# Kernel optimization log

Hardware: AMD Instinct MI355X
Metric: run time of the kernel (lower is better)

## Reference

```python
import jax, jax.numpy as jnp
import numpy as np

B, H, N, D = 4, 16, 4096, 64
M = 266  # nb_features = int(D * ln(D))
KERNEL_EPS = 1e-4


def _gaussian_orthogonal_random_matrix(nb_rows, nb_cols, rng):
    # Faithful to gaussian_orthogonal_random_matrix with scaling=0.
    blocks = []
    for _ in range(nb_rows // nb_cols):
        q, _ = np.linalg.qr(rng.standard_normal((nb_cols, nb_cols)))
        blocks.append(q.T)
    rem = nb_rows - (nb_rows // nb_cols) * nb_cols
    if rem > 0:
        q, _ = np.linalg.qr(rng.standard_normal((nb_cols, nb_cols)))
        blocks.append(q.T[:rem])
    final = np.concatenate(blocks, axis=0)
    mult = np.linalg.norm(rng.standard_normal((nb_rows, nb_cols)), axis=1)
    return (mult[:, None] * final).astype(np.float32)


def setup_inputs() -> dict:
    key = jax.random.key(0)
    kq, kk, kv = jax.random.split(key, 3)
    q = jax.random.normal(kq, (B, H, N, D), dtype=jnp.float32)
    k = jax.random.normal(kk, (B, H, N, D), dtype=jnp.float32)
    v = jax.random.normal(kv, (B, H, N, D), dtype=jnp.float32)
    proj = jnp.asarray(_gaussian_orthogonal_random_matrix(M, D, np.random.default_rng(0)))
    return {"q": q, "k": k, "v": v, "projection_matrix": proj}


def _softmax_kernel(x, proj, is_query):
    d = x.shape[-1]
    data_normalizer = d ** (-0.25)
    ratio = proj.shape[0] ** (-0.5)
    # [b,h,n,m]
    data_dash = jnp.einsum("bhnd,md->bhnm", data_normalizer * x, proj)
    diag = jnp.sum(x * x, axis=-1, keepdims=True) * 0.5 * (data_normalizer ** 2)
    if is_query:
        mx = jax.lax.stop_gradient(jnp.max(data_dash, axis=-1, keepdims=True))
    else:
        mx = jax.lax.stop_gradient(jnp.max(data_dash, axis=(-1, -2), keepdims=True))
    return ratio * (jnp.exp(data_dash - diag - mx) + KERNEL_EPS)


def _linear_attention(q, k, v):
    k_cumsum = jnp.sum(k, axis=-2)                       # [b,h,m]
    D_ = jnp.einsum("bhnm,bhm->bhn", q, k_cumsum)
    D_inv = 1.0 / jnp.where(D_ == 0, 1e-5, D_)
    context = jnp.einsum("bhnm,bhne->bhme", k, v)        # [b,h,m,e]
    return jnp.einsum("bhme,bhnm,bhn->bhne", context, q, D_inv)


def reference(q, k, v, projection_matrix):
    qp = _softmax_kernel(q, projection_matrix, is_query=True)
    kp = _softmax_kernel(k, projection_matrix, is_query=False)
    return _linear_attention(qp, kp, v)
```

## Files before the change

kernel.cpp:

```cpp
#include <hip/hip_runtime.h>
#include <math.h>


#define BH 64
#define NTOK 4096
#define DIM 64
#define MF 266
#define MPAD 272
#define NCH 4
#define CHROWS 1024
#define SUBS 16
#define RATIO 0.06131393394849658f
#define DNORM 0.35355339059327373f
#define DIAGC 0.0625f
#define L2E   1.4426950408889634f
#define KEPS 1e-4f

#define PSTR 72
#define QSTR 296

typedef _Float16 half8 __attribute__((ext_vector_type(8)));
typedef _Float16 half4 __attribute__((ext_vector_type(4)));
typedef __fp16 fp16x2 __attribute__((ext_vector_type(2)));
typedef float floatx4 __attribute__((ext_vector_type(4)));
typedef short short8 __attribute__((ext_vector_type(8)));
typedef short short4s __attribute__((ext_vector_type(4)));

__device__ __forceinline__ short f2h_bits(float f) {
    union { _Float16 h; short s; } u; u.h = (_Float16)f; return u.s;
}
__device__ __forceinline__ float h2f(short s) {
    union { short s; _Float16 h; } u; u.s = s; return (float)u.h;
}
__device__ __forceinline__ unsigned cvt_pk_bf16(float lo, float hi) {
    unsigned r;
    asm("v_cvt_pk_bf16_f32 %0, %1, %2" : "=v"(r) : "v"(lo), "v"(hi));
    return r;
}
__device__ __forceinline__ float fexp2(float x) {
    float r;
    asm("v_exp_f32 %0, %1" : "=v"(r) : "v"(x));
    return r;
}
__device__ __forceinline__ unsigned encf(float f) {
    unsigned u = __float_as_uint(f);
    return (u & 0x80000000u) ? ~u : (u | 0x80000000u);
}
__device__ __forceinline__ float decf(unsigned u) {
    u = (u & 0x80000000u) ? (u & 0x7FFFFFFFu) : ~u;
    return __uint_as_float(u);
}

__global__ __launch_bounds__(512, 4)
void k_pass(const float* __restrict__ kin, const float* __restrict__ vin,
            const float* __restrict__ proj, float* __restrict__ A0p,
            float* __restrict__ S0p, unsigned int* __restrict__ gmax)
{
    __shared__ __align__(16) short kL[2][64 * PSTR];
    __shared__ __align__(16) short vT[2][64 * PSTR];
    __shared__ float diagL[2][64];
    __shared__ __align__(16) short epS[16][16 * PSTR];

    const int tid = threadIdx.x;
    const int l = tid & 63, w = tid >> 6;
    const int c = tid & 15, g = (tid >> 4) & 3;
    const int h    = blockIdx.x >> 8;
    const int rest = blockIdx.x & 255;
    const int bh   = rest >> 2;
    const int ch   = rest & 3;
    const int nT = (h == 1 && w == 0) ? 2 : 1;
    const int t0 = (h == 0) ? w : (8 + w);

    const float PSC = DNORM * L2E;
    half8 pj0[2], pj1[2];
    #pragma unroll
    for (int it = 0; it < 2; ++it) {
        half8 z;
        #pragma unroll
        for (int j = 0; j < 8; ++j) z[j] = (_Float16)0.f;
        pj0[it] = z; pj1[it] = z;
        const int t = it ? 16 : t0;
        const int f = 16 * t + c;
        if (it < nT && f < MF) {
            const float* ps = proj + (size_t)f * 64 + 8 * g;
            float4 x0 = *(const float4*)ps;
            float4 x1 = *(const float4*)(ps + 4);
            float4 x2 = *(const float4*)(ps + 32);
            float4 x3 = *(const float4*)(ps + 36);
            half8 b0, b1;
            b0[0]=(_Float16)(PSC*x0.x); b0[1]=(_Float16)(PSC*x0.y);
            b0[2]=(_Float16)(PSC*x0.z); b0[3]=(_Float16)(PSC*x0.w);
            b0[4]=(_Float16)(PSC*x1.x); b0[5]=(_Float16)(PSC*x1.y);
            b0[6]=(_Float16)(PSC*x1.z); b0[7]=(_Float16)(PSC*x1.w);
            b1[0]=(_Float16)(PSC*x2.x); b1[1]=(_Float16)(PSC*x2.y);
            b1[2]=(_Float16)(PSC*x2.z); b1[3]=(_Float16)(PSC*x2.w);
            b1[4]=(_Float16)(PSC*x3.x); b1[5]=(_Float16)(PSC*x3.y);
            b1[6]=(_Float16)(PSC*x3.z); b1[7]=(_Float16)(PSC*x3.w);
            pj0[it] = b0; pj1[it] = b1;
        }
    }

    const float* kb = kin + ((size_t)bh * NTOK + (size_t)ch * CHROWS) * DIM;
    const float* vb = vin + ((size_t)bh * NTOK + (size_t)ch * CHROWS) * DIM;

    const int srow = 8 * w + (l >> 3);
    const int sd0  = (l & 7) * 8;
    const int vrow = l;
    const int ve0  = 8 * w;

    floatx4 acc[2][4];
    #pragma unroll
    for (int it = 0; it < 2; ++it)
        #pragma unroll
        for (int et = 0; et < 4; ++et) {
            acc[it][et][0]=0.f; acc[it][et][1]=0.f; acc[it][et][2]=0.f; acc[it][et][3]=0.f;
        }
    float s0acc[2] = {0.f, 0.f};
    float dmax = -3.0e38f;

    float4 ka0, ka1, va0, va1;

    auto issue_loads = [&](int s) {
        const float* ks = kb + (size_t)(64 * s + srow) * DIM + sd0;
        ka0 = *(const float4*)ks;
        ka1 = *(const float4*)(ks + 4);
        const float* vs = vb + (size_t)(64 * s + vrow) * DIM + ve0;
        va0 = *(const float4*)vs;
        va1 = *(const float4*)(vs + 4);
    };

    auto stage_write = [&](int buf) {
        union { fp16x2 h2[4]; short8 s8; } uk;
        uk.h2[0] = __builtin_amdgcn_cvt_pkrtz(ka0.x, ka0.y);
        uk.h2[1] = __builtin_amdgcn_cvt_pkrtz(ka0.z, ka0.w);
        uk.h2[2] = __builtin_amdgcn_cvt_pkrtz(ka1.x, ka1.y);
        uk.h2[3] = __builtin_amdgcn_cvt_pkrtz(ka1.z, ka1.w);
        *(short8*)&kL[buf][srow * PSTR + sd0] = uk.s8;
        float ds2 = ka0.x*ka0.x + ka0.y*ka0.y + ka0.z*ka0.z + ka0.w*ka0.w
                  + ka1.x*ka1.x + ka1.y*ka1.y + ka1.z*ka1.z + ka1.w*ka1.w;
        ds2 += __shfl_xor(ds2, 1);
        ds2 += __shfl_xor(ds2, 2);
        ds2 += __shfl_xor(ds2, 4);
        if ((l & 7) == 0) diagL[buf][srow] = ds2 * (DIAGC * L2E);
        unsigned pv0 = cvt_pk_bf16(va0.x, va0.y);
        unsigned pv1 = cvt_pk_bf16(va0.z, va0.w);
        unsigned pv2 = cvt_pk_bf16(va1.x, va1.y);
        unsigned pv3 = cvt_pk_bf16(va1.z, va1.w);
        vT[buf][(ve0 + 0) * PSTR + vrow] = (short)(pv0 & 0xFFFF);
        vT[buf][(ve0 + 1) * PSTR + vrow] = (short)(pv0 >> 16);
        vT[buf][(ve0 + 2) * PSTR + vrow] = (short)(pv1 & 0xFFFF);
        vT[buf][(ve0 + 3) * PSTR + vrow] = (short)(pv1 >> 16);
        vT[buf][(ve0 + 4) * PSTR + vrow] = (short)(pv2 & 0xFFFF);
        vT[buf][(ve0 + 5) * PSTR + vrow] = (short)(pv2 >> 16);
        vT[buf][(ve0 + 6) * PSTR + vrow] = (short)(pv3 & 0xFFFF);
        vT[buf][(ve0 + 7) * PSTR + vrow] = (short)(pv3 >> 16);
    };

    issue_loads(0);
    stage_write(0);
    __syncthreads();

    for (int s = 0; s < SUBS; ++s) {
        const int cur = s & 1;
        const bool more = (s + 1 < SUBS);
        if (more) issue_loads(s + 1);

        #pragma unroll
        for (int nt = 0; nt < 4; ++nt) {
            const half8 a0 = *(const half8*)&kL[cur][(16 * nt + c) * PSTR + 8 * g];
            const half8 a1 = *(const half8*)&kL[cur][(16 * nt + c) * PSTR + 8 * g + 32];
            const float4 dg4 = *(const float4*)&diagL[cur][16 * nt + 4 * g];
            const float dgr[4] = {dg4.x, dg4.y, dg4.z, dg4.w};
            #pragma unroll
            for (int it = 0; it < 2; ++it) {
                if (it < nT) {
                    floatx4 d = {0.f, 0.f, 0.f, 0.f};
                    d = __builtin_amdgcn_mfma_f32_16x16x32_f16(a0, pj0[it], d, 0, 0, 0);
                    d = __builtin_amdgcn_mfma_f32_16x16x32_f16(a1, pj1[it], d, 0, 0, 0);
                    const bool t16 = (it == 1);
                    float ev[4];
                    #pragma unroll
                    for (int r = 0; r < 4; ++r) {
                        const float ddv = d[r];
                        if (!t16 || c < 10) dmax = fmaxf(dmax, ddv);
                        float e = fexp2(ddv - dgr[r]);
                        if (t16 && c == 15) e = 1.0f;
                        s0acc[it] += e;
                        ev[r] = e;
                    }
                    uint2 pk;
                    pk.x = cvt_pk_bf16(ev[0], ev[1]);
                    pk.y = cvt_pk_bf16(ev[2], ev[3]);
                    *(uint2*)&epS[2 * w + it][c * PSTR + 16 * nt + 4 * g] = pk;
                }
            }
        }

        #pragma unroll
        for (int ntp = 0; ntp < 2; ++ntp) {
            const short8 bq0 = *(const short8*)&epS[2 * w][c * PSTR + 32 * ntp + 8 * g];
            short8 bq1;
            if (nT == 2) bq1 = *(const short8*)&epS[2 * w + 1][c * PSTR + 32 * ntp + 8 * g];
            #pragma unroll
            for (int et = 0; et < 4; ++et) {
                const short8 av = *(const short8*)&vT[cur][(16 * et + c) * PSTR + 32 * ntp + 8 * g];
                acc[0][et] = __builtin_amdgcn_mfma_f32_16x16x32_bf16(av, bq0, acc[0][et], 0, 0, 0);
                if (nT == 2)
                    acc[1][et] = __builtin_amdgcn_mfma_f32_16x16x32_bf16(av, bq1, acc[1][et], 0, 0, 0);
            }
        }

        if (more) {
            stage_write(cur ^ 1);
            __syncthreads();
        }
    }

    {
        float* dst = A0p + (size_t)(bh * NCH + ch) * (MPAD * 64);
        #pragma unroll
        for (int it = 0; it < 2; ++it) {
            if (it < nT) {
                const int t = it ? 16 : t0;
                #pragma unroll
                for (int et = 0; et < 4; ++et)
                    *(floatx4*)&dst[(size_t)(16 * t + c) * 64 + 16 * et + 4 * g] = acc[it][et];
            }
        }
    }
    #pragma unroll
    for (int it = 0; it < 2; ++it) {
        if (it < nT) {
            const int t = it ? 16 : t0;
            float s = s0acc[it];
            s += __shfl_xor(s, 16);
            s += __shfl_xor(s, 32);
            if (g == 0 && (t < 16 || c < 10))
                atomicAdd(&S0p[bh * MPAD + 16 * t + c], s);
        }
    }
    #pragma unroll
    for (int sft = 1; sft <= 32; sft <<= 1) dmax = fmaxf(dmax, __shfl_xor(dmax, sft));
    if (l == 0) atomicMax(gmax + bh, encf(dmax));
}

__global__ __launch_bounds__(512, 2)
void reduce_ctx(const float* __restrict__ A0p, const float* __restrict__ S0p,
                const unsigned int* __restrict__ gmax, const float* __restrict__ proj,
                short* __restrict__ ctxw, short* __restrict__ projw)
{
    __shared__ __align__(16) short L[17 * 288];
    const int bh = blockIdx.x >> 2, q = blockIdx.x & 3;
    const int tid = threadIdx.x;
    if (q == 0 && bh < 17) {
        #pragma unroll
        for (int rep = 0; rep < 2; ++rep) {
            const int idx = rep * 512 + tid;
            const int f = 16 * bh + (idx >> 6);
            const int d = idx & 63;
            const float val = (f < MF) ? proj[(size_t)f * 64 + d] * (DNORM * L2E) : 0.f;
            projw[(size_t)f * 64 + d] = f2h_bits(val);
        }
    }
    const float emx = fexp2(-decf(gmax[bh]));
    const int el = tid & 15;
    const int e  = 16 * q + el;
    const int mi = tid >> 4;
    const float* base = A0p + (size_t)bh * NCH * MPAD * 64;
    float vs = 0.f;
    #pragma unroll
    for (int c2 = 0; c2 < NCH; ++c2)
        vs += base[(size_t)c2 * MPAD * 64 + (size_t)271 * 64 + e];
    const float vsr = vs * KEPS;
    for (int m = mi; m < 288; m += 32) {
        float val = 0.f;
        if (m < MF) {
            float s = 0.f;
            #pragma unroll
            for (int c2 = 0; c2 < NCH; ++c2)
                s += base[(size_t)c2 * MPAD * 64 + (size_t)m * 64 + e];
            val = RATIO * (emx * s + vsr);
        }
        L[el * 288 + m] = f2h_bits(val);
    }
    if (q == 0) {
        for (int m = tid; m < 288; m += 512) {
            float val = 0.f;
            if (m < MF) val = RATIO * (emx * S0p[bh * MPAD + m] + KEPS * 4096.0f);
            L[16 * 288 + m] = f2h_bits(val);
        }
    }
    __syncthreads();
    short* dst = ctxw + (size_t)bh * (65 * 288) + (size_t)q * (16 * 288);
    for (int idx = tid; idx < 16 * 36; idx += 512)
        *(short8*)(dst + idx * 8) = *(const short8*)&L[idx * 8];
    if (q == 0) {
        short* kdst = ctxw + (size_t)bh * (65 * 288) + (size_t)64 * 288;
        if (tid < 36)
            *(short8*)(kdst + tid * 8) = *(const short8*)&L[16 * 288 + tid * 8];
    }
}

__global__ __launch_bounds__(512, 2)
void q_pass(const float* __restrict__ qin, const short* __restrict__ projw,
            const short* __restrict__ ctxw, float* __restrict__ outp)
{
    __shared__ __align__(16) short projL[MPAD * PSTR];
    __shared__ __align__(16) short ctxL[65 * QSTR];

    const int tid = threadIdx.x;
    const int bh = blockIdx.x >> 4, rt = blockIdx.x & 15;
    const int c = tid & 15, g = (tid >> 4) & 3, w = tid >> 6;

    for (int idx = tid; idx < MPAD * 8; idx += 512) {
        const int r = idx >> 3, s = idx & 7;
        *(short8*)&projL[r * PSTR + s * 8] = *(const short8*)(projw + (size_t)r * 64 + s * 8);
    }
    {
        const short* src = ctxw + (size_t)bh * (65 * 288);
        for (int idx = tid; idx < 65 * 36; idx += 512) {
            const int r = idx / 36, s = idx - r * 36;
            *(short8*)&ctxL[r * QSTR + s * 8] = *(const short8*)(src + r * 288 + s * 8);
        }
    }
    __syncthreads();

    #pragma unroll 1
    for (int rg = 0; rg < 2; ++rg) {
        const int rowbase = rt * 256 + rg * 128;
        half8 bf0, bf1;
        float dsum = 0.f;
        {
            const float* qs = qin + ((size_t)bh * NTOK + rowbase + 16 * w + c) * DIM;
            #pragma unroll
            for (int ksi = 0; ksi < 2; ++ksi) {
                const float* p4 = qs + ksi * 32 + 8 * g;
                float4 x0 = *(const float4*)p4;
                float4 x1 = *(const float4*)(p4 + 4);
                dsum += x0.x*x0.x + x0.y*x0.y + x0.z*x0.z + x0.w*x0.w
                      + x1.x*x1.x + x1.y*x1.y + x1.z*x1.z + x1.w*x1.w;
                half8& bf = ksi ? bf1 : bf0;
                bf[0]=(_Float16)x0.x; bf[1]=(_Float16)x0.y; bf[2]=(_Float16)x0.z; bf[3]=(_Float16)x0.w;
                bf[4]=(_Float16)x1.x; bf[5]=(_Float16)x1.y; bf[6]=(_Float16)x1.z; bf[7]=(_Float16)x1.w;
            }
        }
        float t1 = dsum + __shfl_xor(dsum, 16);
        const float diagc = (t1 + __shfl_xor(t1, 32)) * (DIAGC * L2E);

        floatx4 dd[17];
        #pragma unroll
        for (int t = 0; t < 17; ++t) {
            const short* ap = &projL[(16 * t + c) * PSTR + 8 * g];
            half8 a0 = *(const half8*)ap;
            half8 a1 = *(const half8*)(ap + 32);
            floatx4 d = {0.f, 0.f, 0.f, 0.f};
            d = __builtin_amdgcn_mfma_f32_16x16x32_f16(a0, bf0, d, 0, 0, 0);
            d = __builtin_amdgcn_mfma_f32_16x16x32_f16(a1, bf1, d, 0, 0, 0);
            dd[t] = d;
        }
        float mx = -3.0e38f;
        #pragma unroll
        for (int t = 0; t < 17; ++t) {
            #pragma unroll
            for (int r2 = 0; r2 < 4; ++r2) {
                const bool fval = (t < 16) || (4 * g + r2 < 10);
                if (fval) mx = fmaxf(mx, dd[t][r2]);
            }
        }
        mx = fmaxf(mx, __shfl_xor(mx, 16));
        mx = fmaxf(mx, __shfl_xor(mx, 32));

        half4 bq[17];
        float denp = 0.f;
        const float sh = diagc + mx;
        #pragma unroll
        for (int t = 0; t < 17; ++t) {
            half4 b;
            #pragma unroll
            for (int r2 = 0; r2 < 4; ++r2) {
                float val = fexp2(dd[t][r2] - sh) + KEPS;
                b[r2] = (_Float16)val;
                denp += val * h2f(ctxL[64 * QSTR + 16 * t + 4 * g + r2]);
            }
            bq[t] = b;
        }
        denp += __shfl_xor(denp, 16);
        denp += __shfl_xor(denp, 32);

        floatx4 acc[4];
        #pragma unroll
        for (int i = 0; i < 4; ++i) { acc[i][0]=0.f; acc[i][1]=0.f; acc[i][2]=0.f; acc[i][3]=0.f; }
        #pragma unroll
        for (int e4 = 0; e4 < 4; ++e4) {
            #pragma unroll
            for (int t = 0; t < 17; ++t) {
                half4 a4 = *(const half4*)&ctxL[(16 * e4 + c) * QSTR + 16 * t + 4 * g];
                acc[e4] = __builtin_amdgcn_mfma_f32_16x16x16f16(a4, bq[t], acc[e4], 0, 0, 0);
            }
        }
        float den = (denp == 0.f) ? 1e-5f : denp;
        const float inv = 1.0f / den;
        float* ob = outp + ((size_t)bh * NTOK + rowbase + 16 * w + c) * DIM;
        #pragma unroll
        for (int e4 = 0; e4 < 4; ++e4) {
            float4 o = make_float4(acc[e4][0] * inv, acc[e4][1] * inv,
                                   acc[e4][2] * inv, acc[e4][3] * inv);
            *(float4*)(ob + 16 * e4 + 4 * g) = o;
        }
    }
}

extern "C" void kernel_launch(void* const* d_in, const int* in_sizes, int n_in,
                              void* d_out, int out_size, void* d_ws, size_t ws_size,
                              hipStream_t stream)
{
    const float* q    = (const float*)d_in[0];
    const float* k    = (const float*)d_in[1];
    const float* v    = (const float*)d_in[2];
    const float* proj = (const float*)d_in[3];
    float* out = (float*)d_out;
    float* ws  = (float*)d_ws;

    const size_t offS = (size_t)BH * NCH * MPAD * 64;
    const size_t offG = offS + (size_t)BH * MPAD;
    const size_t offC = offG + 64;
    const size_t offP = offC + (size_t)BH * 65 * 288 / 2;

    float* A0p = ws;
    float* S0p = ws + offS;
    unsigned int* gmax = (unsigned int*)(ws + offG);
    short* ctxw = (short*)(ws + offC);
    short* projw = (short*)(ws + offP);

    (void)hipMemsetAsync(S0p, 0, ((size_t)BH * MPAD + 64) * sizeof(float), stream);
    hipLaunchKernelGGL(k_pass, dim3(BH * NCH * 2), dim3(512), 0, stream,
                       k, v, proj, A0p, S0p, gmax);
    hipLaunchKernelGGL(reduce_ctx, dim3(BH * 4), dim3(512), 0, stream,
                       A0p, S0p, gmax, proj, ctxw, projw);
    hipLaunchKernelGGL(q_pass, dim3(BH * 16), dim3(512), 0, stream,
                       q, projw, ctxw, out);
}
```

Before: 133.0 us.

## Split K pass into more, smaller chunks and give each Q block one row group

The key/value pass now splits each sequence into 8 chunks of 512 rows instead of 4 of 1024. It stages 32-row sub-tiles with tighter LDS strides and targets 8 blocks per CU through the launch bounds, so more workgroups run at once. The query pass drops its inner two-iteration loop: it launches twice as many blocks, each handling 128 rows, and loads q before the barrier so the load overlaps the context staging. In exchange the number of partial context matrices doubles, which adds workspace writes and reduction traffic in reduce_ctx, and each block does less work to amortise its setup.

```diff
diff --git a/kernel.cpp b/kernel.cpp
--- a/kernel.cpp
+++ b/kernel.cpp
@@ -7,9 +7,10 @@
 #define DIM 64
 #define MF 266
 #define MPAD 272
-#define NCH 4
-#define CHROWS 1024
+#define NCH 8
+#define CHROWS 512
 #define SUBS 16
+#define SUBW 32
 #define RATIO 0.06131393394849658f
 #define DNORM 0.35355339059327373f
 #define DIAGC 0.0625f
@@ -17,6 +18,7 @@
 #define KEPS 1e-4f
 
 #define PSTR 72
+#define ESTR 40
 #define QSTR 296
 
 typedef _Float16 half8 __attribute__((ext_vector_type(8)));
@@ -51,23 +53,23 @@
     return __uint_as_float(u);
 }
 
-__global__ __launch_bounds__(512, 4)
+__global__ __launch_bounds__(512, 8)
 void k_pass(const float* __restrict__ kin, const float* __restrict__ vin,
             const float* __restrict__ proj, float* __restrict__ A0p,
             float* __restrict__ S0p, unsigned int* __restrict__ gmax)
 {
-    __shared__ __align__(16) short kL[2][64 * PSTR];
-    __shared__ __align__(16) short vT[2][64 * PSTR];
-    __shared__ float diagL[2][64];
-    __shared__ __align__(16) short epS[16][16 * PSTR];
+    __shared__ __align__(16) short kL[2][SUBW * PSTR];
+    __shared__ __align__(16) short vT[2][64 * ESTR];
+    __shared__ __align__(16) short epS[9][16 * ESTR];
+    __shared__ float diagL[2][SUBW];
 
     const int tid = threadIdx.x;
     const int l = tid & 63, w = tid >> 6;
-    const int c = tid & 15, g = (tid >> 4) & 3;
-    const int h    = blockIdx.x >> 8;
-    const int rest = blockIdx.x & 255;
-    const int bh   = rest >> 2;
-    const int ch   = rest & 3;
+    const int c = l & 15, g = (l >> 4) & 3;
+    const int h    = blockIdx.x >> 9;
+    const int rest = blockIdx.x & 511;
+    const int bh   = rest >> 3;
+    const int ch   = rest & 7;
     const int nT = (h == 1 && w == 0) ? 2 : 1;
     const int t0 = (h == 0) ? w : (8 + w);
 
@@ -103,10 +105,8 @@
     const float* kb = kin + ((size_t)bh * NTOK + (size_t)ch * CHROWS) * DIM;
     const float* vb = vin + ((size_t)bh * NTOK + (size_t)ch * CHROWS) * DIM;
 
-    const int srow = 8 * w + (l >> 3);
-    const int sd0  = (l & 7) * 8;
-    const int vrow = l;
-    const int ve0  = 8 * w;
+    const int srow = tid >> 4;
+    const int sd0  = (tid & 15) * 4;
 
     floatx4 acc[2][4];
     #pragma unroll
@@ -118,42 +118,35 @@
     float s0acc[2] = {0.f, 0.f};
     float dmax = -3.0e38f;
 
-    float4 ka0, ka1, va0, va1;
+    float4 ka;
+    float vx0, vx1, vx2, vx3;
 
     auto issue_loads = [&](int s) {
-        const float* ks = kb + (size_t)(64 * s + srow) * DIM + sd0;
-        ka0 = *(const float4*)ks;
-        ka1 = *(const float4*)(ks + 4);
-        const float* vs = vb + (size_t)(64 * s + vrow) * DIM + ve0;
-        va0 = *(const float4*)vs;
-        va1 = *(const float4*)(vs + 4);
+        ka = *(const float4*)(kb + (size_t)(SUBW * s + srow) * DIM + sd0);
+        const float* vs = vb + (size_t)(SUBW * s + 4 * w) * DIM + l;
+        vx0 = vs[0];
+        vx1 = vs[64];
+        vx2 = vs[128];
+        vx3 = vs[192];
     };
 
     auto stage_write = [&](int buf) {
-        union { fp16x2 h2[4]; short8 s8; } uk;
-        uk.h2[0] = __builtin_amdgcn_cvt_pkrtz(ka0.x, ka0.y);
-        uk.h2[1] = __builtin_amdgcn_cvt_pkrtz(ka0.z, ka0.w);
-        uk.h2[2] = __builtin_amdgcn_cvt_pkrtz(ka1.x, ka1.y);
-        uk.h2[3] = __builtin_amdgcn_cvt_pkrtz(ka1.z, ka1.w);
-        *(short8*)&kL[buf][srow * PSTR + sd0] = uk.s8;
-        float ds2 = ka0.x*ka0.x + ka0.y*ka0.y + ka0.z*ka0.z + ka0.w*ka0.w
-                  + ka1.x*ka1.x + ka1.y*ka1.y + ka1.z*ka1.z + ka1.w*ka1.w;
+        union { fp16x2 h2[2]; short4s s4; } uk;
+        uk.h2[0] = __builtin_amdgcn_cvt_pkrtz(ka.x, ka.y);
+        uk.h2[1] = __builtin_amdgcn_cvt_pkrtz(ka.z, ka.w);
+        *(short4s*)&kL[buf][srow * PSTR + sd0] = uk.s4;
+        float ds2 = ka.x*ka.x + ka.y*ka.y + ka.z*ka.z + ka.w*ka.w;
         ds2 += __shfl_xor(ds2, 1);
         ds2 += __shfl_xor(ds2, 2);
         ds2 += __shfl_xor(ds2, 4);
-        if ((l & 7) == 0) diagL[buf][srow] = ds2 * (DIAGC * L2E);
-        unsigned pv0 = cvt_pk_bf16(va0.x, va0.y);
-        unsigned pv1 = cvt_pk_bf16(va0.z, va0.w);
-        unsigned pv2 = cvt_pk_bf16(va1.x, va1.y);
-        unsigned pv3 = cvt_pk_bf16(va1.z, va1.w);
-        vT[buf][(ve0 + 0) * PSTR + vrow] = (short)(pv0 & 0xFFFF);
-        vT[buf][(ve0 + 1) * PSTR + vrow] = (short)(pv0 >> 16);
-        vT[buf][(ve0 + 2) * PSTR + vrow] = (short)(pv1 & 0xFFFF);
-        vT[buf][(ve0 + 3) * PSTR + vrow] = (short)(pv1 >> 16);
-        vT[buf][(ve0 + 4) * PSTR + vrow] = (short)(pv2 & 0xFFFF);
-        vT[buf][(ve0 + 5) * PSTR + vrow] = (short)(pv2 >> 16);
-        vT[buf][(ve0 + 6) * PSTR + vrow] = (short)(pv3 & 0xFFFF);
-        vT[buf][(ve0 + 7) * PSTR + vrow] = (short)(pv3 >> 16);
+        ds2 += __shfl_xor(ds2, 8);
+        if ((l & 15) == 0) diagL[buf][srow] = ds2 * (DIAGC * L2E);
+        unsigned pv0 = cvt_pk_bf16(vx0, vx1);
+        unsigned pv1 = cvt_pk_bf16(vx2, vx3);
+        vT[buf][l * ESTR + 4 * w + 0] = (short)(pv0 & 0xFFFF);
+        vT[buf][l * ESTR + 4 * w + 1] = (short)(pv0 >> 16);
+        vT[buf][l * ESTR + 4 * w + 2] = (short)(pv1 & 0xFFFF);
+        vT[buf][l * ESTR + 4 * w + 3] = (short)(pv1 >> 16);
     };
 
     issue_loads(0);
@@ -166,7 +159,7 @@
         if (more) issue_loads(s + 1);
 
         #pragma unroll
-        for (int nt = 0; nt < 4; ++nt) {
+        for (int nt = 0; nt < 2; ++nt) {
             const half8 a0 = *(const half8*)&kL[cur][(16 * nt + c) * PSTR + 8 * g];
             const half8 a1 = *(const half8*)&kL[cur][(16 * nt + c) * PSTR + 8 * g + 32];
             const float4 dg4 = *(const float4*)&diagL[cur][16 * nt + 4 * g];
@@ -191,19 +184,19 @@
                     uint2 pk;
                     pk.x = cvt_pk_bf16(ev[0], ev[1]);
                     pk.y = cvt_pk_bf16(ev[2], ev[3]);
-                    *(uint2*)&epS[2 * w + it][c * PSTR + 16 * nt + 4 * g] = pk;
+                    const int slot = it ? 8 : w;
+                    *(uint2*)&epS[slot][c * ESTR + 16 * nt + 4 * g] = pk;
                 }
             }
         }
 
-        #pragma unroll
-        for (int ntp = 0; ntp < 2; ++ntp) {
-            const short8 bq0 = *(const short8*)&epS[2 * w][c * PSTR + 32 * ntp + 8 * g];
+        {
+            const short8 bq0 = *(const short8*)&epS[w][c * ESTR + 8 * g];
             short8 bq1;
-            if (nT == 2) bq1 = *(const short8*)&epS[2 * w + 1][c * PSTR + 32 * ntp + 8 * g];
+            if (nT == 2) bq1 = *(const short8*)&epS[8][c * ESTR + 8 * g];
             #pragma unroll
             for (int et = 0; et < 4; ++et) {
-                const short8 av = *(const short8*)&vT[cur][(16 * et + c) * PSTR + 32 * ntp + 8 * g];
+                const short8 av = *(const short8*)&vT[cur][(16 * et + c) * ESTR + 8 * g];
                 acc[0][et] = __builtin_amdgcn_mfma_f32_16x16x32_bf16(av, bq0, acc[0][et], 0, 0, 0);
                 if (nT == 2)
                     acc[1][et] = __builtin_amdgcn_mfma_f32_16x16x32_bf16(av, bq1, acc[1][et], 0, 0, 0);
@@ -309,7 +302,7 @@
     __shared__ __align__(16) short ctxL[65 * QSTR];
 
     const int tid = threadIdx.x;
-    const int bh = blockIdx.x >> 4, rt = blockIdx.x & 15;
+    const int bh = blockIdx.x >> 5, rt = blockIdx.x & 31;
     const int c = tid & 15, g = (tid >> 4) & 3, w = tid >> 6;
 
     for (int idx = tid; idx < MPAD * 8; idx += 512) {
@@ -323,90 +316,86 @@
             *(short8*)&ctxL[r * QSTR + s * 8] = *(const short8*)(src + r * 288 + s * 8);
         }
     }
+    half8 bf0, bf1;
+    float dsum = 0.f;
+    {
+        const float* qs = qin + ((size_t)bh * NTOK + rt * 128 + 16 * w + c) * DIM;
+        #pragma unroll
+        for (int ksi = 0; ksi < 2; ++ksi) {
+            const float* p4 = qs + ksi * 32 + 8 * g;
+            float4 x0 = *(const float4*)p4;
+            float4 x1 = *(const float4*)(p4 + 4);
+            dsum += x0.x*x0.x + x0.y*x0.y + x0.z*x0.z + x0.w*x0.w
+                  + x1.x*x1.x + x1.y*x1.y + x1.z*x1.z + x1.w*x1.w;
+            half8& bf = ksi ? bf1 : bf0;
+            bf[0]=(_Float16)x0.x; bf[1]=(_Float16)x0.y; bf[2]=(_Float16)x0.z; bf[3]=(_Float16)x0.w;
+            bf[4]=(_Float16)x1.x; bf[5]=(_Float16)x1.y; bf[6]=(_Float16)x1.z; bf[7]=(_Float16)x1.w;
+        }
+    }
+    float t1 = dsum + __shfl_xor(dsum, 16);
+    const float diagc = (t1 + __shfl_xor(t1, 32)) * (DIAGC * L2E);
+
     __syncthreads();
 
-    #pragma unroll 1
-    for (int rg = 0; rg < 2; ++rg) {
-        const int rowbase = rt * 256 + rg * 128;
-        half8 bf0, bf1;
-        float dsum = 0.f;
-        {
-            const float* qs = qin + ((size_t)bh * NTOK + rowbase + 16 * w + c) * DIM;
-            #pragma unroll
-            for (int ksi = 0; ksi < 2; ++ksi) {
-                const float* p4 = qs + ksi * 32 + 8 * g;
-                float4 x0 = *(const float4*)p4;
-                float4 x1 = *(const float4*)(p4 + 4);
-                dsum += x0.x*x0.x + x0.y*x0.y + x0.z*x0.z + x0.w*x0.w
-                      + x1.x*x1.x + x1.y*x1.y + x1.z*x1.z + x1.w*x1.w;
-                half8& bf = ksi ? bf1 : bf0;
-                bf[0]=(_Float16)x0.x; bf[1]=(_Float16)x0.y; bf[2]=(_Float16)x0.z; bf[3]=(_Float16)x0.w;
-                bf[4]=(_Float16)x1.x; bf[5]=(_Float16)x1.y; bf[6]=(_Float16)x1.z; bf[7]=(_Float16)x1.w;
-            }
-        }
-        float t1 = dsum + __shfl_xor(dsum, 16);
-        const float diagc = (t1 + __shfl_xor(t1, 32)) * (DIAGC * L2E);
-
-        floatx4 dd[17];
+    floatx4 dd[17];
+    #pragma unroll
+    for (int t = 0; t < 17; ++t) {
+        const short* ap = &projL[(16 * t + c) * PSTR + 8 * g];
+        half8 a0 = *(const half8*)ap;
+        half8 a1 = *(const half8*)(ap + 32);
+        floatx4 d = {0.f, 0.f, 0.f, 0.f};
+        d = __builtin_amdgcn_mfma_f32_16x16x32_f16(a0, bf0, d, 0, 0, 0);
+        d = __builtin_amdgcn_mfma_f32_16x16x32_f16(a1, bf1, d, 0, 0, 0);
+        dd[t] = d;
+    }
+    float mx = -3.0e38f;
+    #pragma unroll
+    for (int t = 0; t < 17; ++t) {
+        #pragma unroll
+        for (int r2 = 0; r2 < 4; ++r2) {
+            const bool fval = (t < 16) || (4 * g + r2 < 10);
+            if (fval) mx = fmaxf(mx, dd[t][r2]);
+        }
+    }
+    mx = fmaxf(mx, __shfl_xor(mx, 16));
+    mx = fmaxf(mx, __shfl_xor(mx, 32));
+
+    half4 bq[17];
+    float denp = 0.f;
+    const float sh = diagc + mx;
+    #pragma unroll
+    for (int t = 0; t < 17; ++t) {
+        half4 b;
+        #pragma unroll
+        for (int r2 = 0; r2 < 4; ++r2) {
+            float val = fexp2(dd[t][r2] - sh) + KEPS;
+            b[r2] = (_Float16)val;
+            denp += val * h2f(ctxL[64 * QSTR + 16 * t + 4 * g + r2]);
+        }
+        bq[t] = b;
+    }
+    denp += __shfl_xor(denp, 16);
+    denp += __shfl_xor(denp, 32);
+
+    floatx4 acc[4];
+    #pragma unroll
+    for (int i = 0; i < 4; ++i) { acc[i][0]=0.f; acc[i][1]=0.f; acc[i][2]=0.f; acc[i][3]=0.f; }
+    #pragma unroll
+    for (int e4 = 0; e4 < 4; ++e4) {
         #pragma unroll
         for (int t = 0; t < 17; ++t) {
-            const short* ap = &projL[(16 * t + c) * PSTR + 8 * g];
-            half8 a0 = *(const half8*)ap;
-            half8 a1 = *(const half8*)(ap + 32);
-            floatx4 d = {0.f, 0.f, 0.f, 0.f};
-            d = __builtin_amdgcn_mfma_f32_16x16x32_f16(a0, bf0, d, 0, 0, 0);
-            d = __builtin_amdgcn_mfma_f32_16x16x32_f16(a1, bf1, d, 0, 0, 0);
-            dd[t] = d;
-        }
-        float mx = -3.0e38f;
-        #pragma unroll
-        for (int t = 0; t < 17; ++t) {
-            #pragma unroll
-            for (int r2 = 0; r2 < 4; ++r2) {
-                const bool fval = (t < 16) || (4 * g + r2 < 10);
-                if (fval) mx = fmaxf(mx, dd[t][r2]);
-            }
-        }
-        mx = fmaxf(mx, __shfl_xor(mx, 16));
-        mx = fmaxf(mx, __shfl_xor(mx, 32));
-
-        half4 bq[17];
-        float denp = 0.f;
-        const float sh = diagc + mx;
-        #pragma unroll
-        for (int t = 0; t < 17; ++t) {
-            half4 b;
-            #pragma unroll
-            for (int r2 = 0; r2 < 4; ++r2) {
-                float val = fexp2(dd[t][r2] - sh) + KEPS;
-                b[r2] = (_Float16)val;
-                denp += val * h2f(ctxL[64 * QSTR + 16 * t + 4 * g + r2]);
-            }
-            bq[t] = b;
-        }
-        denp += __shfl_xor(denp, 16);
-        denp += __shfl_xor(denp, 32);
-
-        floatx4 acc[4];
-        #pragma unroll
-        for (int i = 0; i < 4; ++i) { acc[i][0]=0.f; acc[i][1]=0.f; acc[i][2]=0.f; acc[i][3]=0.f; }
-        #pragma unroll
-        for (int e4 = 0; e4 < 4; ++e4) {
-            #pragma unroll
-            for (int t = 0; t < 17; ++t) {
-                half4 a4 = *(const half4*)&ctxL[(16 * e4 + c) * QSTR + 16 * t + 4 * g];
-                acc[e4] = __builtin_amdgcn_mfma_f32_16x16x16f16(a4, bq[t], acc[e4], 0, 0, 0);
-            }
-        }
-        float den = (denp == 0.f) ? 1e-5f : denp;
-        const float inv = 1.0f / den;
-        float* ob = outp + ((size_t)bh * NTOK + rowbase + 16 * w + c) * DIM;
-        #pragma unroll
-        for (int e4 = 0; e4 < 4; ++e4) {
-            float4 o = make_float4(acc[e4][0] * inv, acc[e4][1] * inv,
-                                   acc[e4][2] * inv, acc[e4][3] * inv);
-            *(float4*)(ob + 16 * e4 + 4 * g) = o;
-        }
+            half4 a4 = *(const half4*)&ctxL[(16 * e4 + c) * QSTR + 16 * t + 4 * g];
+            acc[e4] = __builtin_amdgcn_mfma_f32_16x16x16f16(a4, bq[t], acc[e4], 0, 0, 0);
+        }
+    }
+    float den = (denp == 0.f) ? 1e-5f : denp;
+    const float inv = 1.0f / den;
+    float* ob = outp + ((size_t)bh * NTOK + rt * 128 + 16 * w + c) * DIM;
+    #pragma unroll
+    for (int e4 = 0; e4 < 4; ++e4) {
+        float4 o = make_float4(acc[e4][0] * inv, acc[e4][1] * inv,
+                               acc[e4][2] * inv, acc[e4][3] * inv);
+        *(float4*)(ob + 16 * e4 + 4 * g) = o;
     }
 }
 
@@ -437,6 +426,6 @@
                        k, v, proj, A0p, S0p, gmax);
     hipLaunchKernelGGL(reduce_ctx, dim3(BH * 4), dim3(512), 0, stream,
                        A0p, S0p, gmax, proj, ctxw, projw);
-    hipLaunchKernelGGL(q_pass, dim3(BH * 16), dim3(512), 0, stream,
+    hipLaunchKernelGGL(q_pass, dim3(BH * 32), dim3(512), 0, stream,
                        q, projw, ctxw, out);
 }
```

New measurement: 271.3 us. 104% more time.

## Load K fragments directly into MFMA registers and split q_pass into more blocks

Applied to the files above, without the earlier changes.

In k_pass, K is now read from global memory straight into MFMA A-operand registers, and the row norms are computed with shuffles. This removes the kL/diagL shared-memory staging. V is now loaded column-wise so the transposed tile can be written with one vector store. The second projection tile's exp output goes to a single shared slot, which shrinks LDS use. In q_pass each block handles 128 rows instead of looping over 256, doubling the grid to 2048 blocks for more parallelism, at the cost of reloading proj and context into LDS twice as often.

```diff
diff --git a/kernel.cpp b/kernel.cpp
--- a/kernel.cpp
+++ b/kernel.cpp
@@ -56,14 +56,12 @@
             const float* __restrict__ proj, float* __restrict__ A0p,
             float* __restrict__ S0p, unsigned int* __restrict__ gmax)
 {
-    __shared__ __align__(16) short kL[2][64 * PSTR];
     __shared__ __align__(16) short vT[2][64 * PSTR];
-    __shared__ float diagL[2][64];
-    __shared__ __align__(16) short epS[16][16 * PSTR];
+    __shared__ __align__(16) short epS[9][16 * PSTR];
 
     const int tid = threadIdx.x;
     const int l = tid & 63, w = tid >> 6;
-    const int c = tid & 15, g = (tid >> 4) & 3;
+    const int c = l & 15, g = (l >> 4) & 3;
     const int h    = blockIdx.x >> 8;
     const int rest = blockIdx.x & 255;
     const int bh   = rest >> 2;
@@ -103,11 +101,6 @@
     const float* kb = kin + ((size_t)bh * NTOK + (size_t)ch * CHROWS) * DIM;
     const float* vb = vin + ((size_t)bh * NTOK + (size_t)ch * CHROWS) * DIM;
 
-    const int srow = 8 * w + (l >> 3);
-    const int sd0  = (l & 7) * 8;
-    const int vrow = l;
-    const int ve0  = 8 * w;
-
     floatx4 acc[2][4];
     #pragma unroll
     for (int it = 0; it < 2; ++it)
@@ -118,65 +111,61 @@
     float s0acc[2] = {0.f, 0.f};
     float dmax = -3.0e38f;
 
-    float4 ka0, ka1, va0, va1;
-
-    auto issue_loads = [&](int s) {
-        const float* ks = kb + (size_t)(64 * s + srow) * DIM + sd0;
-        ka0 = *(const float4*)ks;
-        ka1 = *(const float4*)(ks + 4);
-        const float* vs = vb + (size_t)(64 * s + vrow) * DIM + ve0;
-        va0 = *(const float4*)vs;
-        va1 = *(const float4*)(vs + 4);
+    float vx[8];
+    auto issue_v = [&](int s) {
+        const float* vs = vb + (size_t)(64 * s + 8 * w) * DIM + l;
+        #pragma unroll
+        for (int i = 0; i < 8; ++i) vx[i] = vs[(size_t)i * DIM];
     };
-
-    auto stage_write = [&](int buf) {
-        union { fp16x2 h2[4]; short8 s8; } uk;
-        uk.h2[0] = __builtin_amdgcn_cvt_pkrtz(ka0.x, ka0.y);
-        uk.h2[1] = __builtin_amdgcn_cvt_pkrtz(ka0.z, ka0.w);
-        uk.h2[2] = __builtin_amdgcn_cvt_pkrtz(ka1.x, ka1.y);
-        uk.h2[3] = __builtin_amdgcn_cvt_pkrtz(ka1.z, ka1.w);
-        *(short8*)&kL[buf][srow * PSTR + sd0] = uk.s8;
-        float ds2 = ka0.x*ka0.x + ka0.y*ka0.y + ka0.z*ka0.z + ka0.w*ka0.w
-                  + ka1.x*ka1.x + ka1.y*ka1.y + ka1.z*ka1.z + ka1.w*ka1.w;
-        ds2 += __shfl_xor(ds2, 1);
-        ds2 += __shfl_xor(ds2, 2);
-        ds2 += __shfl_xor(ds2, 4);
-        if ((l & 7) == 0) diagL[buf][srow] = ds2 * (DIAGC * L2E);
-        unsigned pv0 = cvt_pk_bf16(va0.x, va0.y);
-        unsigned pv1 = cvt_pk_bf16(va0.z, va0.w);
-        unsigned pv2 = cvt_pk_bf16(va1.x, va1.y);
-        unsigned pv3 = cvt_pk_bf16(va1.z, va1.w);
-        vT[buf][(ve0 + 0) * PSTR + vrow] = (short)(pv0 & 0xFFFF);
-        vT[buf][(ve0 + 1) * PSTR + vrow] = (short)(pv0 >> 16);
-        vT[buf][(ve0 + 2) * PSTR + vrow] = (short)(pv1 & 0xFFFF);
-        vT[buf][(ve0 + 3) * PSTR + vrow] = (short)(pv1 >> 16);
-        vT[buf][(ve0 + 4) * PSTR + vrow] = (short)(pv2 & 0xFFFF);
-        vT[buf][(ve0 + 5) * PSTR + vrow] = (short)(pv2 >> 16);
-        vT[buf][(ve0 + 6) * PSTR + vrow] = (short)(pv3 & 0xFFFF);
-        vT[buf][(ve0 + 7) * PSTR + vrow] = (short)(pv3 >> 16);
+    auto stage_v = [&](int buf) {
+        union { unsigned u[4]; short8 s8; } uv;
+        uv.u[0] = cvt_pk_bf16(vx[0], vx[1]);
+        uv.u[1] = cvt_pk_bf16(vx[2], vx[3]);
+        uv.u[2] = cvt_pk_bf16(vx[4], vx[5]);
+        uv.u[3] = cvt_pk_bf16(vx[6], vx[7]);
+        *(short8*)&vT[buf][l * PSTR + 8 * w] = uv.s8;
     };
 
-    issue_loads(0);
-    stage_write(0);
+    issue_v(0);
+    stage_v(0);
     __syncthreads();
 
     for (int s = 0; s < SUBS; ++s) {
         const int cur = s & 1;
         const bool more = (s + 1 < SUBS);
-        if (more) issue_loads(s + 1);
+        if (more) issue_v(s + 1);
 
         #pragma unroll
         for (int nt = 0; nt < 4; ++nt) {
-            const half8 a0 = *(const half8*)&kL[cur][(16 * nt + c) * PSTR + 8 * g];
-            const half8 a1 = *(const half8*)&kL[cur][(16 * nt + c) * PSTR + 8 * g + 32];
-            const float4 dg4 = *(const float4*)&diagL[cur][16 * nt + 4 * g];
-            const float dgr[4] = {dg4.x, dg4.y, dg4.z, dg4.w};
+            const float* kp = kb + (size_t)(64 * s + 16 * nt + c) * DIM + 8 * g;
+            float4 x0 = *(const float4*)kp;
+            float4 x1 = *(const float4*)(kp + 4);
+            float4 x2 = *(const float4*)(kp + 32);
+            float4 x3 = *(const float4*)(kp + 36);
+            float dsum = x0.x*x0.x + x0.y*x0.y + x0.z*x0.z + x0.w*x0.w
+                       + x1.x*x1.x + x1.y*x1.y + x1.z*x1.z + x1.w*x1.w
+                       + x2.x*x2.x + x2.y*x2.y + x2.z*x2.z + x2.w*x2.w
+                       + x3.x*x3.x + x3.y*x3.y + x3.z*x3.z + x3.w*x3.w;
+            float t1 = dsum + __shfl_xor(dsum, 16);
+            const float diagc = (t1 + __shfl_xor(t1, 32)) * (DIAGC * L2E);
+            float dgr[4];
+            #pragma unroll
+            for (int r = 0; r < 4; ++r) dgr[r] = __shfl(diagc, 4 * g + r);
+            union { fp16x2 h2[4]; half8 h8; } ua0, ua1;
+            ua0.h2[0] = __builtin_amdgcn_cvt_pkrtz(x0.x, x0.y);
+            ua0.h2[1] = __builtin_amdgcn_cvt_pkrtz(x0.z, x0.w);
+            ua0.h2[2] = __builtin_amdgcn_cvt_pkrtz(x1.x, x1.y);
+            ua0.h2[3] = __builtin_amdgcn_cvt_pkrtz(x1.z, x1.w);
+            ua1.h2[0] = __builtin_amdgcn_cvt_pkrtz(x2.x, x2.y);
+            ua1.h2[1] = __builtin_amdgcn_cvt_pkrtz(x2.z, x2.w);
+            ua1.h2[2] = __builtin_amdgcn_cvt_pkrtz(x3.x, x3.y);
+            ua1.h2[3] = __builtin_amdgcn_cvt_pkrtz(x3.z, x3.w);
             #pragma unroll
             for (int it = 0; it < 2; ++it) {
                 if (it < nT) {
                     floatx4 d = {0.f, 0.f, 0.f, 0.f};
-                    d = __builtin_amdgcn_mfma_f32_16x16x32_f16(a0, pj0[it], d, 0, 0, 0);
-                    d = __builtin_amdgcn_mfma_f32_16x16x32_f16(a1, pj1[it], d, 0, 0, 0);
+                    d = __builtin_amdgcn_mfma_f32_16x16x32_f16(ua0.h8, pj0[it], d, 0, 0, 0);
+                    d = __builtin_amdgcn_mfma_f32_16x16x32_f16(ua1.h8, pj1[it], d, 0, 0, 0);
                     const bool t16 = (it == 1);
                     float ev[4];
                     #pragma unroll
@@ -191,16 +180,17 @@
                     uint2 pk;
                     pk.x = cvt_pk_bf16(ev[0], ev[1]);
                     pk.y = cvt_pk_bf16(ev[2], ev[3]);
-                    *(uint2*)&epS[2 * w + it][c * PSTR + 16 * nt + 4 * g] = pk;
+                    const int slot = it ? 8 : w;
+                    *(uint2*)&epS[slot][c * PSTR + 16 * nt + 4 * g] = pk;
                 }
             }
         }
 
         #pragma unroll
         for (int ntp = 0; ntp < 2; ++ntp) {
-            const short8 bq0 = *(const short8*)&epS[2 * w][c * PSTR + 32 * ntp + 8 * g];
+            const short8 bq0 = *(const short8*)&epS[w][c * PSTR + 32 * ntp + 8 * g];
             short8 bq1;
-            if (nT == 2) bq1 = *(const short8*)&epS[2 * w + 1][c * PSTR + 32 * ntp + 8 * g];
+            if (nT == 2) bq1 = *(const short8*)&epS[8][c * PSTR + 32 * ntp + 8 * g];
             #pragma unroll
             for (int et = 0; et < 4; ++et) {
                 const short8 av = *(const short8*)&vT[cur][(16 * et + c) * PSTR + 32 * ntp + 8 * g];
@@ -211,7 +201,7 @@
         }
 
         if (more) {
-            stage_write(cur ^ 1);
+            stage_v(cur ^ 1);
             __syncthreads();
         }
     }
@@ -309,7 +299,7 @@
     __shared__ __align__(16) short ctxL[65 * QSTR];
 
     const int tid = threadIdx.x;
-    const int bh = blockIdx.x >> 4, rt = blockIdx.x & 15;
+    const int bh = blockIdx.x >> 5, rt = blockIdx.x & 31;
     const int c = tid & 15, g = (tid >> 4) & 3, w = tid >> 6;
 
     for (int idx = tid; idx < MPAD * 8; idx += 512) {
@@ -323,90 +313,86 @@
             *(short8*)&ctxL[r * QSTR + s * 8] = *(const short8*)(src + r * 288 + s * 8);
         }
     }
+    half8 bf0, bf1;
+    float dsum = 0.f;
+    {
+        const float* qs = qin + ((size_t)bh * NTOK + rt * 128 + 16 * w + c) * DIM;
+        #pragma unroll
+        for (int ksi = 0; ksi < 2; ++ksi) {
+            const float* p4 = qs + ksi * 32 + 8 * g;
+            float4 x0 = *(const float4*)p4;
+            float4 x1 = *(const float4*)(p4 + 4);
+            dsum += x0.x*x0.x + x0.y*x0.y + x0.z*x0.z + x0.w*x0.w
+                  + x1.x*x1.x + x1.y*x1.y + x1.z*x1.z + x1.w*x1.w;
+            half8& bf = ksi ? bf1 : bf0;
+            bf[0]=(_Float16)x0.x; bf[1]=(_Float16)x0.y; bf[2]=(_Float16)x0.z; bf[3]=(_Float16)x0.w;
+            bf[4]=(_Float16)x1.x; bf[5]=(_Float16)x1.y; bf[6]=(_Float16)x1.z; bf[7]=(_Float16)x1.w;
+        }
+    }
+    float t1 = dsum + __shfl_xor(dsum, 16);
+    const float diagc = (t1 + __shfl_xor(t1, 32)) * (DIAGC * L2E);
+
     __syncthreads();
 
-    #pragma unroll 1
-    for (int rg = 0; rg < 2; ++rg) {
-        const int rowbase = rt * 256 + rg * 128;
-        half8 bf0, bf1;
-        float dsum = 0.f;
-        {
-            const float* qs = qin + ((size_t)bh * NTOK + rowbase + 16 * w + c) * DIM;
-            #pragma unroll
-            for (int ksi = 0; ksi < 2; ++ksi) {
-                const float* p4 = qs + ksi * 32 + 8 * g;
-                float4 x0 = *(const float4*)p4;
-                float4 x1 = *(const float4*)(p4 + 4);
-                dsum += x0.x*x0.x + x0.y*x0.y + x0.z*x0.z + x0.w*x0.w
-                      + x1.x*x1.x + x1.y*x1.y + x1.z*x1.z + x1.w*x1.w;
-                half8& bf = ksi ? bf1 : bf0;
-                bf[0]=(_Float16)x0.x; bf[1]=(_Float16)x0.y; bf[2]=(_Float16)x0.z; bf[3]=(_Float16)x0.w;
-                bf[4]=(_Float16)x1.x; bf[5]=(_Float16)x1.y; bf[6]=(_Float16)x1.z; bf[7]=(_Float16)x1.w;
-            }
-        }
-        float t1 = dsum + __shfl_xor(dsum, 16);
-        const float diagc = (t1 + __shfl_xor(t1, 32)) * (DIAGC * L2E);
-
-        floatx4 dd[17];
+    floatx4 dd[17];
+    #pragma unroll
+    for (int t = 0; t < 17; ++t) {
+        const short* ap = &projL[(16 * t + c) * PSTR + 8 * g];
+        half8 a0 = *(const half8*)ap;
+        half8 a1 = *(const half8*)(ap + 32);
+        floatx4 d = {0.f, 0.f, 0.f, 0.f};
+        d = __builtin_amdgcn_mfma_f32_16x16x32_f16(a0, bf0, d, 0, 0, 0);
+        d = __builtin_amdgcn_mfma_f32_16x16x32_f16(a1, bf1, d, 0, 0, 0);
+        dd[t] = d;
+    }
+    float mx = -3.0e38f;
+    #pragma unroll
+    for (int t = 0; t < 17; ++t) {
+        #pragma unroll
+        for (int r2 = 0; r2 < 4; ++r2) {
+            const bool fval = (t < 16) || (4 * g + r2 < 10);
+            if (fval) mx = fmaxf(mx, dd[t][r2]);
+        }
+    }
+    mx = fmaxf(mx, __shfl_xor(mx, 16));
+    mx = fmaxf(mx, __shfl_xor(mx, 32));
+
+    half4 bq[17];
+    float denp = 0.f;
+    const float sh = diagc + mx;
+    #pragma unroll
+    for (int t = 0; t < 17; ++t) {
+        half4 b;
+        #pragma unroll
+        for (int r2 = 0; r2 < 4; ++r2) {
+            float val = fexp2(dd[t][r2] - sh) + KEPS;
+            b[r2] = (_Float16)val;
+            denp += val * h2f(ctxL[64 * QSTR + 16 * t + 4 * g + r2]);
+        }
+        bq[t] = b;
+    }
+    denp += __shfl_xor(denp, 16);
+    denp += __shfl_xor(denp, 32);
+
+    floatx4 acc[4];
+    #pragma unroll
+    for (int i = 0; i < 4; ++i) { acc[i][0]=0.f; acc[i][1]=0.f; acc[i][2]=0.f; acc[i][3]=0.f; }
+    #pragma unroll
+    for (int e4 = 0; e4 < 4; ++e4) {
         #pragma unroll
         for (int t = 0; t < 17; ++t) {
-            const short* ap = &projL[(16 * t + c) * PSTR + 8 * g];
-            half8 a0 = *(const half8*)ap;
-            half8 a1 = *(const half8*)(ap + 32);
-            floatx4 d = {0.f, 0.f, 0.f, 0.f};
-            d = __builtin_amdgcn_mfma_f32_16x16x32_f16(a0, bf0, d, 0, 0, 0);
-            d = __builtin_amdgcn_mfma_f32_16x16x32_f16(a1, bf1, d, 0, 0, 0);
-            dd[t] = d;
-        }
-        float mx = -3.0e38f;
-        #pragma unroll
-        for (int t = 0; t < 17; ++t) {
-            #pragma unroll
-            for (int r2 = 0; r2 < 4; ++r2) {
-                const bool fval = (t < 16) || (4 * g + r2 < 10);
-                if (fval) mx = fmaxf(mx, dd[t][r2]);
-            }
-        }
-        mx = fmaxf(mx, __shfl_xor(mx, 16));
-        mx = fmaxf(mx, __shfl_xor(mx, 32));
-
-        half4 bq[17];
-        float denp = 0.f;
-        const float sh = diagc + mx;
-        #pragma unroll
-        for (int t = 0; t < 17; ++t) {
-            half4 b;
-            #pragma unroll
-            for (int r2 = 0; r2 < 4; ++r2) {
-                float val = fexp2(dd[t][r2] - sh) + KEPS;
-                b[r2] = (_Float16)val;
-                denp += val * h2f(ctxL[64 * QSTR + 16 * t + 4 * g + r2]);
-            }
-            bq[t] = b;
-        }
-        denp += __shfl_xor(denp, 16);
-        denp += __shfl_xor(denp, 32);
-
-        floatx4 acc[4];
-        #pragma unroll
-        for (int i = 0; i < 4; ++i) { acc[i][0]=0.f; acc[i][1]=0.f; acc[i][2]=0.f; acc[i][3]=0.f; }
-        #pragma unroll
-        for (int e4 = 0; e4 < 4; ++e4) {
-            #pragma unroll
-            for (int t = 0; t < 17; ++t) {
-                half4 a4 = *(const half4*)&ctxL[(16 * e4 + c) * QSTR + 16 * t + 4 * g];
-                acc[e4] = __builtin_amdgcn_mfma_f32_16x16x16f16(a4, bq[t], acc[e4], 0, 0, 0);
-            }
-        }
-        float den = (denp == 0.f) ? 1e-5f : denp;
-        const float inv = 1.0f / den;
-        float* ob = outp + ((size_t)bh * NTOK + rowbase + 16 * w + c) * DIM;
-        #pragma unroll
-        for (int e4 = 0; e4 < 4; ++e4) {
-            float4 o = make_float4(acc[e4][0] * inv, acc[e4][1] * inv,
-                                   acc[e4][2] * inv, acc[e4][3] * inv);
-            *(float4*)(ob + 16 * e4 + 4 * g) = o;
-        }
+            half4 a4 = *(const half4*)&ctxL[(16 * e4 + c) * QSTR + 16 * t + 4 * g];
+            acc[e4] = __builtin_amdgcn_mfma_f32_16x16x16f16(a4, bq[t], acc[e4], 0, 0, 0);
+        }
+    }
+    float den = (denp == 0.f) ? 1e-5f : denp;
+    const float inv = 1.0f / den;
+    float* ob = outp + ((size_t)bh * NTOK + rt * 128 + 16 * w + c) * DIM;
+    #pragma unroll
+    for (int e4 = 0; e4 < 4; ++e4) {
+        float4 o = make_float4(acc[e4][0] * inv, acc[e4][1] * inv,
+                               acc[e4][2] * inv, acc[e4][3] * inv);
+        *(float4*)(ob + 16 * e4 + 4 * g) = o;
     }
 }
 
@@ -437,6 +423,6 @@
                        k, v, proj, A0p, S0p, gmax);
     hipLaunchKernelGGL(reduce_ctx, dim3(BH * 4), dim3(512), 0, stream,
                        A0p, S0p, gmax, proj, ctxw, projw);
-    hipLaunchKernelGGL(q_pass, dim3(BH * 16), dim3(512), 0, stream,
+    hipLaunchKernelGGL(q_pass, dim3(BH * 32), dim3(512), 0, stream,
                        q, projw, ctxw, out);
 }
```

Measured after the change: 215.2 us. +61.8%, slower.
